# Kernel optimization log

Hardware: AMD Instinct MI355X
Metric: run time of the kernel (lower is better)

The kernel has to match this reference:

```python
import math
import jax, jax.numpy as jnp
import numpy as np

N_BLOCKS = 8
D_MODEL = 1024
D_FF = 4096
B, T = 4, 2048
EPS = 1e-5


def setup_inputs() -> dict:
    key = jax.random.key(0)
    ks = jax.random.split(key, 8)
    s = 0.02  # small init so deep stack stays numerically sane
    return {
        "x": jax.random.normal(ks[0], (B, T, D_MODEL), jnp.float32),
        "ln1_w": jnp.ones((N_BLOCKS, D_MODEL), jnp.float32),
        "ln1_b": jnp.zeros((N_BLOCKS, D_MODEL), jnp.float32),
        "qkv_w": jax.random.normal(ks[1], (N_BLOCKS, 3 * D_MODEL, D_MODEL), jnp.float32) * s,
        "qkv_b": jnp.zeros((N_BLOCKS, 3 * D_MODEL), jnp.float32),
        "out_w": jax.random.normal(ks[2], (N_BLOCKS, D_MODEL, D_MODEL), jnp.float32) * s,
        "out_b": jnp.zeros((N_BLOCKS, D_MODEL), jnp.float32),
        "ln2_w": jnp.ones((N_BLOCKS, D_MODEL), jnp.float32),
        "ln2_b": jnp.zeros((N_BLOCKS, D_MODEL), jnp.float32),
        "ff0_w": jax.random.normal(ks[3], (N_BLOCKS, D_FF, D_MODEL), jnp.float32) * s,
        "ff0_b": jnp.zeros((N_BLOCKS, D_FF), jnp.float32),
        "ff3_w": jax.random.normal(ks[4], (N_BLOCKS, D_MODEL, D_FF), jnp.float32) * s,
        "ff3_b": jnp.zeros((N_BLOCKS, D_MODEL), jnp.float32),
    }


def _layer_norm(x, w, b):
    mean = jnp.mean(x, axis=-1, keepdims=True)
    var = jnp.mean(jnp.square(x - mean), axis=-1, keepdims=True)
    return (x - mean) / jnp.sqrt(var + EPS) * w + b


def reference(x, ln1_w, ln1_b, qkv_w, qkv_b, out_w, out_b,
              ln2_w, ln2_b, ff0_w, ff0_b, ff3_w, ff3_b):
    Bq, Tq, C = x.shape
    scale = 1.0 / math.sqrt(C)
    mask = jnp.triu(jnp.ones((Tq, Tq), bool), k=1)  # True above diagonal -> masked

    def block(xc, p):
        l1w, l1b, qw, qb, ow, ob, l2w, l2b, f0w, f0b, f3w, f3b = p
        h = _layer_norm(xc, l1w, l1b)
        qkv = h @ qw.T + qb  # [B,T,3C]
        q, k, v = jnp.split(qkv, 3, axis=-1)
        att = jnp.einsum('btc,bsc->bts', q, k) * scale
        att = jnp.where(mask, -jnp.inf, att)
        att = jax.nn.softmax(att, axis=-1)
        out = jnp.einsum('bts,bsc->btc', att, v)
        xc = xc + out @ ow.T + ob
        h2 = _layer_norm(xc, l2w, l2b)
        ff = jax.nn.gelu(h2 @ f0w.T + f0b, approximate=False)
        xc = xc + ff @ f3w.T + f3b
        return xc, None

    params = (ln1_w, ln1_b, qkv_w, qkv_b, out_w, out_b,
              ln2_w, ln2_b, ff0_w, ff0_b, ff3_w, ff3_b)
    x, _ = jax.lax.scan(block, x, params)
    return x
```

## Files before the change

### kernel.cpp

```cpp
#include <hip/hip_runtime.h>
#include <hip/hip_bf16.h>
#include <math.h>


typedef __bf16 bf16;
typedef __bf16 bf16x8 __attribute__((ext_vector_type(8)));
typedef __bf16 bf16x4 __attribute__((ext_vector_type(4)));
typedef float f32x4 __attribute__((ext_vector_type(4)));

#define BM 128
#define BN 128
#define BK 32

__device__ __forceinline__ void async_load16(const void* g, void* l) {
  __builtin_amdgcn_global_load_lds(
      (const __attribute__((address_space(1))) void*)g,
      (__attribute__((address_space(3))) void*)l, 16, 0, 0);
}

constexpr int EPI_BF16 = 0;
constexpr int EPI_GELU = 1;
constexpr int EPI_RESID = 2;
constexpr int EPI_F32SCALE = 3;

template <int EPI>
__global__ __launch_bounds__(256) void gemm_bt(
    const bf16* __restrict__ A, const bf16* __restrict__ Bw,
    const float* __restrict__ bias, const float* __restrict__ resid,
    void* __restrict__ Cout, int K, int lda, int ldb, int ldc,
    long batchA, long batchB, long batchC, float alpha,
    int causalSkip, int kLimit) {
  const int m0 = blockIdx.y * BM;
  const int n0 = blockIdx.x * BN;
  if (causalSkip && n0 > m0) return;
  const int bz = blockIdx.z;
  const bf16* Ab = A + (long)bz * batchA;
  const bf16* Bb = Bw + (long)bz * batchB;
  const int kEnd = kLimit ? ((m0 + BM < K) ? (m0 + BM) : K) : K;

  __shared__ bf16 As[BM * BK];
  __shared__ bf16 Bs[BN * BK];

  const int tid = threadIdx.x;
  const int wave = tid >> 6;
  const int lane = tid & 63;
  const int wr = wave >> 1;
  const int wc = wave & 1;
  const int l16 = lane & 15;
  const int kq = (lane >> 4) * 8;

  f32x4 acc[4][4] = {};

  for (int k0 = 0; k0 < kEnd; k0 += BK) {
#pragma unroll
    for (int rep = 0; rep < 2; rep++) {
      const int c = tid + rep * 256;
      const int r = c >> 2;
      const int ck = (c & 3) << 3;
      const bf16* gA = Ab + (long)(m0 + r) * lda + (k0 + ck);
      const bf16* gB = Bb + (long)(n0 + r) * ldb + (k0 + ck);
      bf16* lA = As + (c & ~63) * 8;
      bf16* lB = Bs + (c & ~63) * 8;
      async_load16(gA, lA);
      async_load16(gB, lB);
    }
    __syncthreads();
    bf16x8 af[4], bfr[4];
#pragma unroll
    for (int i = 0; i < 4; i++)
      af[i] = *(const bf16x8*)(As + (wr * 64 + i * 16 + l16) * BK + kq);
#pragma unroll
    for (int j = 0; j < 4; j++)
      bfr[j] = *(const bf16x8*)(Bs + (wc * 64 + j * 16 + l16) * BK + kq);
#pragma unroll
    for (int i = 0; i < 4; i++)
#pragma unroll
      for (int j = 0; j < 4; j++)
        acc[i][j] = __builtin_amdgcn_mfma_f32_16x16x32_bf16(af[i], bfr[j],
                                                            acc[i][j], 0, 0, 0);
    __syncthreads();
  }

  const int baseRow = m0 + wr * 64 + (lane >> 4) * 4;
  const int baseCol = n0 + wc * 64 + l16;
#pragma unroll
  for (int j = 0; j < 4; j++) {
    const int col = baseCol + j * 16;
    float bv = 0.0f;
    if (EPI != EPI_F32SCALE && bias != nullptr) bv = bias[col];
#pragma unroll
    for (int i = 0; i < 4; i++) {
      const int row0 = baseRow + i * 16;
#pragma unroll
      for (int r = 0; r < 4; r++) {
        const float v = acc[i][j][r];
        const long idx = (long)bz * batchC + (long)(row0 + r) * ldc + col;
        if (EPI == EPI_F32SCALE) {
          ((float*)Cout)[idx] = v * alpha;
        } else if (EPI == EPI_RESID) {
          ((float*)Cout)[idx] = resid[idx] + v + bv;
        } else if (EPI == EPI_GELU) {
          const float u = v + bv;
          const float g = 0.5f * u * (1.0f + erff(u * 0.70710678118654752f));
          ((bf16*)Cout)[idx] = (bf16)g;
        } else {
          ((bf16*)Cout)[idx] = (bf16)(v + bv);
        }
      }
    }
  }
}

__global__ __launch_bounds__(256) void ln_kernel(
    const float* __restrict__ x, const float* __restrict__ w,
    const float* __restrict__ b, bf16* __restrict__ out) {
  const int C = 1024;
  const long row = blockIdx.x;
  const int t = threadIdx.x;
  const float4 v = ((const float4*)(x + row * C))[t];
  float s = v.x + v.y + v.z + v.w;
  float sq = v.x * v.x + v.y * v.y + v.z * v.z + v.w * v.w;
#pragma unroll
  for (int o = 1; o < 64; o <<= 1) {
    s += __shfl_xor(s, o, 64);
    sq += __shfl_xor(sq, o, 64);
  }
  __shared__ float rs[4], rq[4];
  const int wv = t >> 6, ln = t & 63;
  if (!ln) { rs[wv] = s; rq[wv] = sq; }
  __syncthreads();
  s = rs[0] + rs[1] + rs[2] + rs[3];
  sq = rq[0] + rq[1] + rq[2] + rq[3];
  const float mean = s * (1.0f / 1024.0f);
  const float var = sq * (1.0f / 1024.0f) - mean * mean;
  const float rstd = rsqrtf(var + 1e-5f);
  const float4 wv4 = ((const float4*)w)[t];
  const float4 bv4 = ((const float4*)b)[t];
  bf16x4 o = {(bf16)((v.x - mean) * rstd * wv4.x + bv4.x),
              (bf16)((v.y - mean) * rstd * wv4.y + bv4.y),
              (bf16)((v.z - mean) * rstd * wv4.z + bv4.z),
              (bf16)((v.w - mean) * rstd * wv4.w + bv4.w)};
  ((bf16x4*)(out + row * C))[t] = o;
}

__global__ __launch_bounds__(256) void softmax_causal(
    const float* __restrict__ S, bf16* __restrict__ P) {
  const int T = 2048;
  const int t = blockIdx.x, b = blockIdx.y;
  const long rowoff = ((long)b * T + t) * (long)T;
  const float* row = S + rowoff;
  bf16* prow = P + rowoff;
  const int L = t + 1;
  const int tid = threadIdx.x;
  float vals[8];
  float mx = -1e30f;
#pragma unroll
  for (int i = 0; i < 8; i++) {
    const int idx = tid + i * 256;
    if (idx < L) {
      vals[i] = row[idx];
      mx = fmaxf(mx, vals[i]);
    } else {
      vals[i] = -1e30f;
    }
  }
#pragma unroll
  for (int o = 1; o < 64; o <<= 1) mx = fmaxf(mx, __shfl_xor(mx, o, 64));
  __shared__ float red[4], red2[4];
  const int wv = tid >> 6, ln = tid & 63;
  if (!ln) red[wv] = mx;
  __syncthreads();
  mx = fmaxf(fmaxf(red[0], red[1]), fmaxf(red[2], red[3]));
  float sum = 0.0f;
#pragma unroll
  for (int i = 0; i < 8; i++) {
    const int idx = tid + i * 256;
    const float e = (idx < L) ? __expf(vals[i] - mx) : 0.0f;
    vals[i] = e;
    sum += e;
  }
#pragma unroll
  for (int o = 1; o < 64; o <<= 1) sum += __shfl_xor(sum, o, 64);
  if (!ln) red2[wv] = sum;
  __syncthreads();
  sum = red2[0] + red2[1] + red2[2] + red2[3];
  const float inv = 1.0f / sum;
#pragma unroll
  for (int i = 0; i < 8; i++) prow[tid + i * 256] = (bf16)(vals[i] * inv);
}

__global__ __launch_bounds__(256) void transpose_v(
    const bf16* __restrict__ qkv, bf16* __restrict__ vt) {
  const int T = 2048, C3 = 3072, C = 1024, COFF = 2048;
  __shared__ bf16 tile[32][33];
  const int b = blockIdx.z;
  const int s0 = blockIdx.x * 32, c0 = blockIdx.y * 32;
  const int tx = threadIdx.x & 31, ty0 = threadIdx.x >> 5;
#pragma unroll
  for (int j = 0; j < 4; j++) {
    const int ty = ty0 + j * 8;
    tile[ty][tx] = qkv[((long)b * T + s0 + ty) * C3 + COFF + c0 + tx];
  }
  __syncthreads();
#pragma unroll
  for (int j = 0; j < 4; j++) {
    const int ty = ty0 + j * 8;
    vt[(long)b * C * T + (long)(c0 + ty) * T + s0 + tx] = tile[tx][ty];
  }
}

__global__ void f2bf_kernel(const float* __restrict__ in,
                            bf16* __restrict__ out, long n4) {
  const long i = (long)blockIdx.x * blockDim.x + threadIdx.x;
  if (i < n4) {
    const float4 v = ((const float4*)in)[i];
    bf16x4 o = {(bf16)v.x, (bf16)v.y, (bf16)v.z, (bf16)v.w};
    ((bf16x4*)out)[i] = o;
  }
}

extern "C" void kernel_launch(void* const* d_in, const int* in_sizes, int n_in,
                              void* d_out, int out_size, void* d_ws,
                              size_t ws_size, hipStream_t stream) {
  const int Bb = 4, T = 2048, C = 1024, FF = 4096, NB = 8;
  const int M = Bb * T;
  const float* x_in = (const float*)d_in[0];
  const float* ln1_w = (const float*)d_in[1];
  const float* ln1_b = (const float*)d_in[2];
  const float* qkv_w = (const float*)d_in[3];
  const float* qkv_b = (const float*)d_in[4];
  const float* out_w = (const float*)d_in[5];
  const float* out_b = (const float*)d_in[6];
  const float* ln2_w = (const float*)d_in[7];
  const float* ln2_b = (const float*)d_in[8];
  const float* ff0_w = (const float*)d_in[9];
  const float* ff0_b = (const float*)d_in[10];
  const float* ff3_w = (const float*)d_in[11];
  const float* ff3_b = (const float*)d_in[12];
  float* x = (float*)d_out;

  char* p = (char*)d_ws;
  auto alloc = [&](size_t bytes) {
    char* r = p;
    p += (bytes + 255) & ~(size_t)255;
    return r;
  };
  bf16* wqkv = (bf16*)alloc((size_t)NB * 3 * C * C * 2);
  bf16* wout = (bf16*)alloc((size_t)NB * C * C * 2);
  bf16* wff0 = (bf16*)alloc((size_t)NB * FF * C * 2);
  bf16* wff3 = (bf16*)alloc((size_t)NB * C * FF * 2);
  bf16* hbuf = (bf16*)alloc((size_t)M * C * 2);
  bf16* qkvb = (bf16*)alloc((size_t)M * 3 * C * 2);
  float* att = (float*)alloc((size_t)Bb * T * T * 4);
  bf16* pbuf = (bf16*)alloc((size_t)Bb * T * T * 2);
  bf16* vt = (bf16*)alloc((size_t)Bb * C * T * 2);
  bf16* aout = (bf16*)alloc((size_t)M * C * 2);
  bf16* ffb = (bf16*)att;

  auto conv = [&](const float* src, bf16* dst, long n) {
    const long n4 = n / 4;
    f2bf_kernel<<<dim3((unsigned)((n4 + 255) / 256)), dim3(256), 0, stream>>>(
        src, dst, n4);
  };
  conv(qkv_w, wqkv, (long)NB * 3 * C * C);
  conv(out_w, wout, (long)NB * C * C);
  conv(ff0_w, wff0, (long)NB * FF * C);
  conv(ff3_w, wff3, (long)NB * C * FF);

  hipMemcpyAsync(x, x_in, (size_t)M * C * 4, hipMemcpyDeviceToDevice, stream);

  const float scale = 1.0f / 32.0f;

  for (int blk = 0; blk < NB; blk++) {
    const bf16* wq = wqkv + (long)blk * 3 * C * C;
    const bf16* wo = wout + (long)blk * C * C;
    const bf16* w0 = wff0 + (long)blk * FF * C;
    const bf16* w3 = wff3 + (long)blk * C * FF;
    const float* l1w = ln1_w + blk * C;
    const float* l1b = ln1_b + blk * C;
    const float* l2w = ln2_w + blk * C;
    const float* l2b = ln2_b + blk * C;
    const float* qb = qkv_b + blk * 3 * C;
    const float* ob = out_b + blk * C;
    const float* f0b = ff0_b + blk * FF;
    const float* f3b = ff3_b + blk * C;

    ln_kernel<<<dim3(M), dim3(256), 0, stream>>>(x, l1w, l1b, hbuf);
    gemm_bt<EPI_BF16><<<dim3(3 * C / BN, M / BM), dim3(256), 0, stream>>>(
        hbuf, wq, qb, nullptr, qkvb, C, C, C, 3 * C, 0, 0, 0, 1.0f, 0, 0);
    gemm_bt<EPI_F32SCALE><<<dim3(T / BN, T / BM, Bb), dim3(256), 0, stream>>>(
        qkvb, qkvb + C, nullptr, nullptr, att, C, 3 * C, 3 * C, T,
        (long)T * 3 * C, (long)T * 3 * C, (long)T * T, scale, 1, 0);
    softmax_causal<<<dim3(T, Bb), dim3(256), 0, stream>>>(att, pbuf);
    transpose_v<<<dim3(T / 32, C / 32, Bb), dim3(256), 0, stream>>>(qkvb, vt);
    gemm_bt<EPI_BF16><<<dim3(C / BN, T / BM, Bb), dim3(256), 0, stream>>>(
        pbuf, vt, nullptr, nullptr, aout, T, T, T, C, (long)T * T, (long)C * T,
        (long)T * C, 1.0f, 0, 1);
    gemm_bt<EPI_RESID><<<dim3(C / BN, M / BM), dim3(256), 0, stream>>>(
        aout, wo, ob, x, x, C, C, C, C, 0, 0, 0, 1.0f, 0, 0);
    ln_kernel<<<dim3(M), dim3(256), 0, stream>>>(x, l2w, l2b, hbuf);
    gemm_bt<EPI_GELU><<<dim3(FF / BN, M / BM), dim3(256), 0, stream>>>(
        hbuf, w0, f0b, nullptr, ffb, C, C, C, FF, 0, 0, 0, 1.0f, 0, 0);
    gemm_bt<EPI_RESID><<<dim3(C / BN, M / BM), dim3(256), 0, stream>>>(
        ffb, w3, f3b, x, x, FF, FF, FF, C, 0, 0, 0, 1.0f, 0, 0);
  }
}
```

Measured before the change: 4.582 ms.

## Swizzle GEMM LDS layout, remap tiles per XCD, hoist load address math

The GEMM now XOR-swizzles the 16-byte chunk position when staging A/B tiles into LDS and applies the matching swizzle on fragment reads, which should reduce LDS bank conflicts. Block indices are remapped so consecutive M-tiles go to the same XCD, improving L2 reuse of the shared B/A tiles. Global and LDS addresses are precomputed outside the K loop and a min-blocks-per-CU hint of 4 is added. The remap assumes the M-tile count is a multiple of 8, and the occupancy hint may push the compiler toward register spills.

```diff
diff --git a/kernel.cpp b/kernel.cpp
--- a/kernel.cpp
+++ b/kernel.cpp
@@ -24,14 +24,20 @@
 constexpr int EPI_F32SCALE = 3;
 
 template <int EPI>
-__global__ __launch_bounds__(256) void gemm_bt(
+__global__ __launch_bounds__(256, 4) void gemm_bt(
     const bf16* __restrict__ A, const bf16* __restrict__ Bw,
     const float* __restrict__ bias, const float* __restrict__ resid,
     void* __restrict__ Cout, int K, int lda, int ldb, int ldc,
     long batchA, long batchB, long batchC, float alpha,
     int causalSkip, int kLimit) {
-  const int m0 = blockIdx.y * BM;
-  const int n0 = blockIdx.x * BN;
+  const int nx = gridDim.x;
+  const int lin = blockIdx.y * nx + blockIdx.x;
+  const int xcd = lin & 7;
+  const int t = lin >> 3;
+  const int n_idx = t % nx;
+  const int j_idx = t / nx;
+  const int m0 = (xcd + 8 * j_idx) * BM;
+  const int n0 = n_idx * BN;
   if (causalSkip && n0 > m0) return;
   const int bz = blockIdx.z;
   const bf16* Ab = A + (long)bz * batchA;
@@ -47,31 +53,48 @@
   const int wr = wave >> 1;
   const int wc = wave & 1;
   const int l16 = lane & 15;
-  const int kq = (lane >> 4) * 8;
+  const int kq = lane >> 4;
+
+  const bf16* gAp[2];
+  const bf16* gBp[2];
+  bf16* lAp[2];
+  bf16* lBp[2];
+#pragma unroll
+  for (int rep = 0; rep < 2; rep++) {
+    const int c = tid + rep * 256;
+    const int r = c >> 2;
+    const int qc = (c & 3) ^ ((r >> 1) & 3);
+    gAp[rep] = Ab + (long)(m0 + r) * lda + qc * 8;
+    gBp[rep] = Bb + (long)(n0 + r) * ldb + qc * 8;
+    lAp[rep] = As + (c & ~63) * 8;
+    lBp[rep] = Bs + (c & ~63) * 8;
+  }
+
+  const int swz = (l16 >> 1) & 3;
+  const int kqs = (kq ^ swz) * 8;
+  int offA[4], offB[4];
+#pragma unroll
+  for (int i = 0; i < 4; i++) {
+    offA[i] = (wr * 64 + i * 16 + l16) * BK + kqs;
+    offB[i] = (wc * 64 + i * 16 + l16) * BK + kqs;
+  }
 
   f32x4 acc[4][4] = {};
 
   for (int k0 = 0; k0 < kEnd; k0 += BK) {
 #pragma unroll
     for (int rep = 0; rep < 2; rep++) {
-      const int c = tid + rep * 256;
-      const int r = c >> 2;
-      const int ck = (c & 3) << 3;
-      const bf16* gA = Ab + (long)(m0 + r) * lda + (k0 + ck);
-      const bf16* gB = Bb + (long)(n0 + r) * ldb + (k0 + ck);
-      bf16* lA = As + (c & ~63) * 8;
-      bf16* lB = Bs + (c & ~63) * 8;
-      async_load16(gA, lA);
-      async_load16(gB, lB);
+      async_load16(gAp[rep], lAp[rep]);
+      async_load16(gBp[rep], lBp[rep]);
+      gAp[rep] += BK;
+      gBp[rep] += BK;
     }
     __syncthreads();
     bf16x8 af[4], bfr[4];
 #pragma unroll
-    for (int i = 0; i < 4; i++)
-      af[i] = *(const bf16x8*)(As + (wr * 64 + i * 16 + l16) * BK + kq);
-#pragma unroll
-    for (int j = 0; j < 4; j++)
-      bfr[j] = *(const bf16x8*)(Bs + (wc * 64 + j * 16 + l16) * BK + kq);
+    for (int i = 0; i < 4; i++) af[i] = *(const bf16x8*)(As + offA[i]);
+#pragma unroll
+    for (int j = 0; j < 4; j++) bfr[j] = *(const bf16x8*)(Bs + offB[j]);
 #pragma unroll
     for (int i = 0; i < 4; i++)
 #pragma unroll
```

Result: faster. 4.077 ms (-11.0%).
